# Kernel tuning notes

Hardware: AMD Instinct MI355X
Metric: run time of the kernel (lower is better)

## Reference

```python
import jax, jax.numpy as jnp
import numpy as np


def setup_inputs() -> dict:
    key = jax.random.key(0)
    k1, k2, k3, k4 = jax.random.split(key, 4)
    B, C, H, W = 32, 2048, 24, 24
    MID = 256
    cam = jax.random.normal(k1, (B, C, H, W), dtype=jnp.float32)
    feat = jax.random.normal(k2, (B, C, H, W), dtype=jnp.float32)
    # 1x1 conv weights (no bias): [out_ch, in_ch]
    W1 = jax.random.normal(k3, (MID, C), dtype=jnp.float32) * (1.0 / np.sqrt(C))
    W2 = jax.random.normal(k4, (MID, C), dtype=jnp.float32) * (1.0 / np.sqrt(C))
    alpha = jnp.ones((), dtype=jnp.float32)
    return {"cam": cam, "feat": feat, "W1": W1, "W2": W2, "alpha": alpha}


def reference(cam, feat, W1, W2, alpha):
    B, C, H, W = cam.shape
    N = H * W
    feat_flat = feat.reshape(B, C, N)            # b c n
    f1 = jnp.einsum('mc,bcn->bmn', W1, feat_flat)  # 1x1 conv == channel GEMM
    f2 = jnp.einsum('mc,bcn->bmn', W2, feat_flat)
    attn = jnp.einsum('bmi,bmj->bij', f1, f2)    # b n n
    attn = jax.nn.softmax(attn, axis=-1)
    cam_flat = cam.reshape(B, C, N).transpose(0, 2, 1)  # b n c
    cam_refined = jnp.einsum('bij,bjc->bic', attn, cam_flat)  # b n c
    cam_refined = cam_refined.transpose(0, 2, 1).reshape(B, C, H, W)
    return alpha * cam_refined + cam
```

## Files before the change

### kernel.cpp

```cpp
#include <hip/hip_runtime.h>
#include <math.h>

typedef unsigned short u16;
typedef unsigned int u32;
typedef _Float16 f16;
typedef __attribute__((ext_vector_type(8))) _Float16 f16x8;
typedef __attribute__((ext_vector_type(4))) float f32x4;

static constexpr int B_   = 32;
static constexpr int C_   = 2048;
static constexpr int N_   = 576;
static constexpr int MID_ = 256;
static constexpr int M_   = 512;
static constexpr int NB_  = B_ * N_;

typedef const __attribute__((address_space(1))) unsigned int gu32_t;
typedef __attribute__((address_space(3))) unsigned int lu32_t;
__device__ __forceinline__ void gl16(const void* g, void* l) {
  __builtin_amdgcn_global_load_lds((gu32_t*)g, (lu32_t*)l, 16, 0, 0);
}

__global__ __launch_bounds__(256) void k_prep_w(
    const float* __restrict__ W1, const float* __restrict__ W2,
    f16* __restrict__ Wc) {
  const int e0 = (blockIdx.x * 256 + threadIdx.x) * 8;
  const int m = e0 >> 11;
  const int c = e0 & 2047;
  const float* src = (m < MID_) ? &W1[(size_t)m * C_ + c]
                                : &W2[(size_t)(m - MID_) * C_ + c];
  const float4 a = *(const float4*)&src[0];
  const float4 b = *(const float4*)&src[4];
  f16x8 hv;
  hv[0] = (f16)a.x; hv[1] = (f16)a.y; hv[2] = (f16)a.z; hv[3] = (f16)a.w;
  hv[4] = (f16)b.x; hv[5] = (f16)b.y; hv[6] = (f16)b.z; hv[7] = (f16)b.w;
  *(f16x8*)&Wc[e0] = hv;
}

__global__ __launch_bounds__(256) void k_prep_feat(
    const float* __restrict__ feat, f16* __restrict__ fT) {
  const int c0 = blockIdx.x * 64;
  const int n0 = blockIdx.y * 64;
  const int b  = blockIdx.z;
  __shared__ float Ts[64][65];
  const float* src = feat + ((size_t)b * C_ + c0) * N_ + n0;
  const int t = threadIdx.x;
  const int tr  = t >> 4;
  const int tc4 = (t & 15) * 4;
#pragma unroll
  for (int e = 0; e < 4; ++e) {
    const int c = tr + e * 16;
    const float4 v = *(const float4*)&src[(size_t)c * N_ + tc4];
    Ts[c][tc4] = v.x; Ts[c][tc4 + 1] = v.y;
    Ts[c][tc4 + 2] = v.z; Ts[c][tc4 + 3] = v.w;
  }
  __syncthreads();
  const int co = (t & 7) * 8;
#pragma unroll
  for (int p = 0; p < 2; ++p) {
    const int n = (t >> 3) + p * 32;
    f16x8 hv;
#pragma unroll
    for (int e = 0; e < 8; ++e) hv[e] = (f16)Ts[co + e][n];
    *(f16x8*)&fT[((size_t)b * N_ + n0 + n) * C_ + c0 + co] = hv;
  }
}

__global__ __launch_bounds__(256) void k_prep_cam(
    const float* __restrict__ cam, f16* __restrict__ camh) {
  const int e0 = (blockIdx.x * 256 + threadIdx.x) * 8;
  const float4 a = *(const float4*)&cam[e0];
  const float4 b = *(const float4*)&cam[e0 + 4];
  f16x8 hv;
  hv[0] = (f16)a.x; hv[1] = (f16)a.y; hv[2] = (f16)a.z; hv[3] = (f16)a.w;
  hv[4] = (f16)b.x; hv[5] = (f16)b.y; hv[6] = (f16)b.z; hv[7] = (f16)b.w;
  *(f16x8*)&camh[e0] = hv;
}

__global__ __launch_bounds__(256) void k_f12(
    const f16* __restrict__ fT, const f16* __restrict__ Wc,
    f16* __restrict__ f12) {
  const int mt = blockIdx.x;
  const int nt = blockIdx.y;
  __shared__ __align__(16) f16 As[128 * 32], Bs[128 * 32];
  const int t = threadIdx.x, lane = t & 63, w = t >> 6;
  const int wm = (w >> 1) * 64, wn = (w & 1) * 64;
  const int n0 = nt * 128, m0 = mt * 128;
  const int rrow = lane >> 2;
  const int koff = (lane & 3) * 8;
  const int r0 = w * 32;

  f32x4 acc[4][4];
#pragma unroll
  for (int i = 0; i < 4; ++i)
#pragma unroll
    for (int j = 0; j < 4; ++j) acc[i][j] = (f32x4)(0.0f);

  for (int k0 = 0; k0 < C_; k0 += 32) {
#pragma unroll
    for (int q = 0; q < 2; ++q) {
      const int row = r0 + q * 16 + rrow;
      const int lb = (r0 + q * 16) * 32;
      gl16(&fT[(size_t)(n0 + row) * C_ + k0 + koff], &As[lb]);
      gl16(&Wc[(size_t)(m0 + row) * C_ + k0 + koff], &Bs[lb]);
    }
    __syncthreads();
    const int fr = lane & 15, qo = (lane >> 4) * 8;
    f16x8 af[4], bf[4];
#pragma unroll
    for (int i = 0; i < 4; ++i) {
      af[i] = *(const f16x8*)&As[(wm + 16 * i + fr) * 32 + qo];
      bf[i] = *(const f16x8*)&Bs[(wn + 16 * i + fr) * 32 + qo];
    }
#pragma unroll
    for (int i = 0; i < 4; ++i)
#pragma unroll
      for (int j = 0; j < 4; ++j)
        acc[i][j] = __builtin_amdgcn_mfma_f32_16x16x32_f16(af[i], bf[j], acc[i][j], 0, 0, 0);
    __syncthreads();
  }
#pragma unroll
  for (int i = 0; i < 4; ++i) {
    const int nb = n0 + wm + 16 * i + ((lane >> 4) * 4);
#pragma unroll
    for (int j = 0; j < 4; ++j) {
      const int m = m0 + wn + 16 * j + (lane & 15);
#pragma unroll
      for (int r = 0; r < 4; ++r)
        f12[(size_t)(nb + r) * M_ + m] = (f16)acc[i][j][r];
    }
  }
}

__global__ __launch_bounds__(256) void k_logits(
    const f16* __restrict__ f12, float* __restrict__ logits) {
  const int jt = blockIdx.x;
  const int it = blockIdx.y;
  const int b  = blockIdx.z;
  __shared__ __align__(16) f16 As[128 * 32], Bs[128 * 32];
  const int t = threadIdx.x, lane = t & 63, w = t >> 6;
  const int wm = (w >> 1) * 64, wn = (w & 1) * 64;
  const int i0 = it * 128, j0 = jt * 128;
  const int rrow = lane >> 2;
  const int koff = (lane & 3) * 8;
  const int r0 = w * 32;
  const f16* f_b = f12 + (size_t)b * N_ * M_;

  f32x4 acc[4][4];
#pragma unroll
  for (int i = 0; i < 4; ++i)
#pragma unroll
    for (int j = 0; j < 4; ++j) acc[i][j] = (f32x4)(0.0f);

  for (int k0 = 0; k0 < MID_; k0 += 32) {
#pragma unroll
    for (int q = 0; q < 2; ++q) {
      const int row = r0 + q * 16 + rrow;
      const int ig = min(i0 + row, N_ - 1);
      const int jg = min(j0 + row, N_ - 1);
      const int lb = (r0 + q * 16) * 32;
      gl16(&f_b[(size_t)ig * M_ + k0 + koff], &As[lb]);
      gl16(&f_b[(size_t)jg * M_ + MID_ + k0 + koff], &Bs[lb]);
    }
    __syncthreads();
    const int fr = lane & 15, qo = (lane >> 4) * 8;
    f16x8 af[4], bf[4];
#pragma unroll
    for (int i = 0; i < 4; ++i) {
      af[i] = *(const f16x8*)&As[(wm + 16 * i + fr) * 32 + qo];
      bf[i] = *(const f16x8*)&Bs[(wn + 16 * i + fr) * 32 + qo];
    }
#pragma unroll
    for (int i = 0; i < 4; ++i)
#pragma unroll
      for (int j = 0; j < 4; ++j)
        acc[i][j] = __builtin_amdgcn_mfma_f32_16x16x32_f16(af[i], bf[j], acc[i][j], 0, 0, 0);
    __syncthreads();
  }
  float* log_b = logits + (size_t)b * N_ * N_;
#pragma unroll
  for (int i = 0; i < 4; ++i) {
    const int ibase = i0 + wm + 16 * i + ((lane >> 4) * 4);
#pragma unroll
    for (int j = 0; j < 4; ++j) {
      const int jj = j0 + wn + 16 * j + (lane & 15);
      if (jj < N_) {
#pragma unroll
        for (int r = 0; r < 4; ++r) {
          const int ii = ibase + r;
          if (ii < N_) log_b[(size_t)ii * N_ + jj] = acc[i][j][r];
        }
      }
    }
  }
}

__global__ __launch_bounds__(64) void k_softmax(
    const float* __restrict__ logits, f16* __restrict__ attn) {
  const int row = blockIdx.x;
  const float* p = logits + (size_t)row * N_;
  f16* o = attn + (size_t)row * N_;
  const int lane = threadIdx.x;
  float v[9];
  float mx = -INFINITY;
#pragma unroll
  for (int q = 0; q < 9; ++q) {
    v[q] = p[lane + q * 64];
    mx = fmaxf(mx, v[q]);
  }
#pragma unroll
  for (int off = 32; off > 0; off >>= 1) mx = fmaxf(mx, __shfl_down(mx, off));
  mx = __shfl(mx, 0);
  float s = 0.f;
#pragma unroll
  for (int q = 0; q < 9; ++q) {
    v[q] = __expf(v[q] - mx);
    s += v[q];
  }
#pragma unroll
  for (int off = 32; off > 0; off >>= 1) s += __shfl_down(s, off);
  s = __shfl(s, 0);
  const float inv = 1.0f / s;
#pragma unroll
  for (int q = 0; q < 9; ++q) o[lane + q * 64] = (f16)(v[q] * inv);
}

__global__ __launch_bounds__(256) void k_out(
    const f16* __restrict__ camh, const f16* __restrict__ attn,
    const float* __restrict__ alpha_p, float* __restrict__ out) {
  const int ct = blockIdx.x;
  const int it = blockIdx.y;
  const int b  = blockIdx.z;
  __shared__ __align__(16) f16 As[128 * 32], Bs[128 * 32];
  const int t = threadIdx.x, lane = t & 63, w = t >> 6;
  const int wm = (w >> 1) * 64, wn = (w & 1) * 64;
  const int c0 = ct * 128, i0 = it * 128;
  const int rrow = lane >> 2;
  const int koff = (lane & 3) * 8;
  const int r0 = w * 32;
  const f16* camh_b = camh + (size_t)b * C_ * N_;
  const f16* attn_b = attn + (size_t)b * N_ * N_;

  f32x4 acc[4][4];
#pragma unroll
  for (int i = 0; i < 4; ++i)
#pragma unroll
    for (int j = 0; j < 4; ++j) acc[i][j] = (f32x4)(0.0f);

  for (int k0 = 0; k0 < N_; k0 += 32) {
#pragma unroll
    for (int q = 0; q < 2; ++q) {
      const int row = r0 + q * 16 + rrow;
      const int cg = c0 + row;
      const int ig = min(i0 + row, N_ - 1);
      const int lb = (r0 + q * 16) * 32;
      gl16(&camh_b[(size_t)cg * N_ + k0 + koff], &As[lb]);
      gl16(&attn_b[(size_t)ig * N_ + k0 + koff], &Bs[lb]);
    }
    __syncthreads();
    const int fr = lane & 15, qo = (lane >> 4) * 8;
    f16x8 af[4], bf[4];
#pragma unroll
    for (int i = 0; i < 4; ++i) {
      af[i] = *(const f16x8*)&As[(wm + 16 * i + fr) * 32 + qo];
      bf[i] = *(const f16x8*)&Bs[(wn + 16 * i + fr) * 32 + qo];
    }
#pragma unroll
    for (int i = 0; i < 4; ++i)
#pragma unroll
      for (int j = 0; j < 4; ++j)
        acc[i][j] = __builtin_amdgcn_mfma_f32_16x16x32_f16(af[i], bf[j], acc[i][j], 0, 0, 0);
    __syncthreads();
  }
  const float alpha = *alpha_p;
  float* out_b = out + (size_t)b * C_ * N_;
#pragma unroll
  for (int ii = 0; ii < 4; ++ii) {
    const int c = c0 + wm + 16 * ii + ((lane >> 4) * 4);
#pragma unroll
    for (int jj = 0; jj < 4; ++jj) {
      const int i = i0 + wn + 16 * jj + (lane & 15);
      if (i < N_) {
#pragma unroll
        for (int r = 0; r < 4; ++r) {
          const size_t off = (size_t)(c + r) * N_ + i;
          out_b[off] = alpha * acc[ii][jj][r] + (float)camh_b[off];
        }
      }
    }
  }
}

extern "C" void kernel_launch(void* const* d_in, const int* in_sizes, int n_in,
                              void* d_out, int out_size, void* d_ws,
                              size_t ws_size, hipStream_t stream) {
  const float* cam   = (const float*)d_in[0];
  const float* feat  = (const float*)d_in[1];
  const float* W1    = (const float*)d_in[2];
  const float* W2    = (const float*)d_in[3];
  const float* alpha = (const float*)d_in[4];
  float* out = (float*)d_out;

  char* ws = (char*)d_ws;
  f16*   fT     = (f16*)ws;
  f16*   f12    = (f16*)(ws + 75497472);
  f16*   Wc     = (f16*)(ws + 94371840);
  float* logits = (float*)ws;
  f16*   attn   = (f16*)(ws + 75497472);
  f16*   camh   = (f16*)ws;

  k_prep_w<<<dim3(512), 256, 0, stream>>>(W1, W2, Wc);
  k_prep_feat<<<dim3(32, 9, B_), 256, 0, stream>>>(feat, fT);
  k_f12<<<dim3(4, 144), 256, 0, stream>>>(fT, Wc, f12);
  k_logits<<<dim3(5, 5, B_), 256, 0, stream>>>(f12, logits);
  k_softmax<<<dim3(B_ * N_), 64, 0, stream>>>(logits, attn);
  k_prep_cam<<<dim3(18432), 256, 0, stream>>>(cam, camh);
  k_out<<<dim3(16, 5, B_), 256, 0, stream>>>(camh, attn, alpha, out);
}
```

Baseline: 531.2 us.

## Fuse cam fp16 conversion into output GEMM, swizzle LDS, batch softmax rows

Drops the separate cam-to-fp16 kernel. The output GEMM now loads fp32 cam directly, converts it in registers and writes it to LDS, and the residual add reads fp32 cam instead of the fp16 copy. It also XOR-swizzles the LDS k-offsets in all three GEMMs to reduce bank conflicts, and packs four softmax rows into each 256-thread block. The fused path removes one full read-write pass over cam, but loses the async global-to-LDS load for the A tile, and cam is read twice as many bytes per tile.

```diff
diff --git a/kernel.cpp b/kernel.cpp
--- a/kernel.cpp
+++ b/kernel.cpp
@@ -19,6 +19,7 @@
 __device__ __forceinline__ void gl16(const void* g, void* l) {
   __builtin_amdgcn_global_load_lds((gu32_t*)g, (lu32_t*)l, 16, 0, 0);
 }
+
 
 __global__ __launch_bounds__(256) void k_prep_w(
     const float* __restrict__ W1, const float* __restrict__ W2,
@@ -65,17 +66,6 @@
   }
 }
 
-__global__ __launch_bounds__(256) void k_prep_cam(
-    const float* __restrict__ cam, f16* __restrict__ camh) {
-  const int e0 = (blockIdx.x * 256 + threadIdx.x) * 8;
-  const float4 a = *(const float4*)&cam[e0];
-  const float4 b = *(const float4*)&cam[e0 + 4];
-  f16x8 hv;
-  hv[0] = (f16)a.x; hv[1] = (f16)a.y; hv[2] = (f16)a.z; hv[3] = (f16)a.w;
-  hv[4] = (f16)b.x; hv[5] = (f16)b.y; hv[6] = (f16)b.z; hv[7] = (f16)b.w;
-  *(f16x8*)&camh[e0] = hv;
-}
-
 __global__ __launch_bounds__(256) void k_f12(
     const f16* __restrict__ fT, const f16* __restrict__ Wc,
     f16* __restrict__ f12) {
@@ -86,8 +76,10 @@
   const int wm = (w >> 1) * 64, wn = (w & 1) * 64;
   const int n0 = nt * 128, m0 = mt * 128;
   const int rrow = lane >> 2;
-  const int koff = (lane & 3) * 8;
+  const int koff = ((lane & 3) ^ ((lane >> 3) & 3)) * 8;
   const int r0 = w * 32;
+  const int fr = lane & 15;
+  const int qo = (((lane >> 4) ^ ((lane >> 1) & 3)) * 8);
 
   f32x4 acc[4][4];
 #pragma unroll
@@ -104,7 +96,6 @@
       gl16(&Wc[(size_t)(m0 + row) * C_ + k0 + koff], &Bs[lb]);
     }
     __syncthreads();
-    const int fr = lane & 15, qo = (lane >> 4) * 8;
     f16x8 af[4], bf[4];
 #pragma unroll
     for (int i = 0; i < 4; ++i) {
@@ -141,8 +132,10 @@
   const int wm = (w >> 1) * 64, wn = (w & 1) * 64;
   const int i0 = it * 128, j0 = jt * 128;
   const int rrow = lane >> 2;
-  const int koff = (lane & 3) * 8;
+  const int koff = ((lane & 3) ^ ((lane >> 3) & 3)) * 8;
   const int r0 = w * 32;
+  const int fr = lane & 15;
+  const int qo = (((lane >> 4) ^ ((lane >> 1) & 3)) * 8);
   const f16* f_b = f12 + (size_t)b * N_ * M_;
 
   f32x4 acc[4][4];
@@ -162,7 +155,6 @@
       gl16(&f_b[(size_t)jg * M_ + MID_ + k0 + koff], &Bs[lb]);
     }
     __syncthreads();
-    const int fr = lane & 15, qo = (lane >> 4) * 8;
     f16x8 af[4], bf[4];
 #pragma unroll
     for (int i = 0; i < 4; ++i) {
@@ -194,12 +186,12 @@
   }
 }
 
-__global__ __launch_bounds__(64) void k_softmax(
+__global__ __launch_bounds__(256) void k_softmax(
     const float* __restrict__ logits, f16* __restrict__ attn) {
-  const int row = blockIdx.x;
+  const int row = blockIdx.x * 4 + (threadIdx.x >> 6);
+  const int lane = threadIdx.x & 63;
   const float* p = logits + (size_t)row * N_;
   f16* o = attn + (size_t)row * N_;
-  const int lane = threadIdx.x;
   float v[9];
   float mx = -INFINITY;
 #pragma unroll
@@ -225,7 +217,7 @@
 }
 
 __global__ __launch_bounds__(256) void k_out(
-    const f16* __restrict__ camh, const f16* __restrict__ attn,
+    const float* __restrict__ cam, const f16* __restrict__ attn,
     const float* __restrict__ alpha_p, float* __restrict__ out) {
   const int ct = blockIdx.x;
   const int it = blockIdx.y;
@@ -235,9 +227,11 @@
   const int wm = (w >> 1) * 64, wn = (w & 1) * 64;
   const int c0 = ct * 128, i0 = it * 128;
   const int rrow = lane >> 2;
-  const int koff = (lane & 3) * 8;
+  const int koff = ((lane & 3) ^ ((lane >> 3) & 3)) * 8;
   const int r0 = w * 32;
-  const f16* camh_b = camh + (size_t)b * C_ * N_;
+  const int fr = lane & 15;
+  const int qo = (((lane >> 4) ^ ((lane >> 1) & 3)) * 8);
+  const float* cam_b = cam + (size_t)b * C_ * N_;
   const f16* attn_b = attn + (size_t)b * N_ * N_;
 
   f32x4 acc[4][4];
@@ -247,17 +241,28 @@
     for (int j = 0; j < 4; ++j) acc[i][j] = (f32x4)(0.0f);
 
   for (int k0 = 0; k0 < N_; k0 += 32) {
+    float4 a0[2], a1[2];
 #pragma unroll
     for (int q = 0; q < 2; ++q) {
       const int row = r0 + q * 16 + rrow;
-      const int cg = c0 + row;
       const int ig = min(i0 + row, N_ - 1);
       const int lb = (r0 + q * 16) * 32;
-      gl16(&camh_b[(size_t)cg * N_ + k0 + koff], &As[lb]);
       gl16(&attn_b[(size_t)ig * N_ + k0 + koff], &Bs[lb]);
-    }
-    __syncthreads();
-    const int fr = lane & 15, qo = (lane >> 4) * 8;
+      const float* s = &cam_b[(size_t)(c0 + row) * N_ + k0 + koff];
+      a0[q] = *(const float4*)&s[0];
+      a1[q] = *(const float4*)&s[4];
+    }
+#pragma unroll
+    for (int q = 0; q < 2; ++q) {
+      const int lb = (r0 + q * 16) * 32;
+      f16x8 hv;
+      hv[0] = (f16)a0[q].x; hv[1] = (f16)a0[q].y;
+      hv[2] = (f16)a0[q].z; hv[3] = (f16)a0[q].w;
+      hv[4] = (f16)a1[q].x; hv[5] = (f16)a1[q].y;
+      hv[6] = (f16)a1[q].z; hv[7] = (f16)a1[q].w;
+      *(f16x8*)&As[lb + lane * 8] = hv;
+    }
+    __syncthreads();
     f16x8 af[4], bf[4];
 #pragma unroll
     for (int i = 0; i < 4; ++i) {
@@ -283,7 +288,7 @@
 #pragma unroll
         for (int r = 0; r < 4; ++r) {
           const size_t off = (size_t)(c + r) * N_ + i;
-          out_b[off] = alpha * acc[ii][jj][r] + (float)camh_b[off];
+          out_b[off] = alpha * acc[ii][jj][r] + cam_b[off];
         }
       }
     }
@@ -306,13 +311,11 @@
   f16*   Wc     = (f16*)(ws + 94371840);
   float* logits = (float*)ws;
   f16*   attn   = (f16*)(ws + 75497472);
-  f16*   camh   = (f16*)ws;
 
   k_prep_w<<<dim3(512), 256, 0, stream>>>(W1, W2, Wc);
   k_prep_feat<<<dim3(32, 9, B_), 256, 0, stream>>>(feat, fT);
   k_f12<<<dim3(4, 144), 256, 0, stream>>>(fT, Wc, f12);
   k_logits<<<dim3(5, 5, B_), 256, 0, stream>>>(f12, logits);
-  k_softmax<<<dim3(B_ * N_), 64, 0, stream>>>(logits, attn);
-  k_prep_cam<<<dim3(18432), 256, 0, stream>>>(cam, camh);
-  k_out<<<dim3(16, 5, B_), 256, 0, stream>>>(camh, attn, alpha, out);
-}
+  k_softmax<<<dim3(NB_ / 4), 256, 0, stream>>>(logits, attn);
+  k_out<<<dim3(16, 5, B_), 256, 0, stream>>>(cam, attn, alpha, out);
+}
```

Result: no change. 541.8 us (+2.0%).
